# Kernel optimization log

Measured on AMD Instinct MI355X. Metric: run time of the kernel, lower is better.

The kernel has to match this reference:

```python
import jax, jax.numpy as jnp
import numpy as np

B, T, S, H, V, L = 64, 60, 60, 512, 32000, 2
NEG = -1.0e9  # matches torch mask value -1000000000.0


def setup_inputs() -> dict:
    key = jax.random.key(0)
    ks = jax.random.split(key, 12)
    sc = 0.05
    return {
        "indices": jax.random.randint(ks[0], (B, T), 0, V),
        "enc_output": jax.random.normal(ks[1], (B, S, H), dtype=jnp.float32),
        "de_lens": jax.random.randint(ks[2], (B,), 1, S + 1),
        "emb": jax.random.normal(ks[3], (V, H), dtype=jnp.float32) * sc,
        "w_ih": jax.random.normal(ks[4], (L, 4 * H, H), dtype=jnp.float32) * sc,
        "w_hh": jax.random.normal(ks[5], (L, 4 * H, H), dtype=jnp.float32) * sc,
        "b_ih": jnp.zeros((L, 4 * H), dtype=jnp.float32),
        "b_hh": jnp.zeros((L, 4 * H), dtype=jnp.float32),
        "lin_w": jax.random.normal(ks[6], (L, H, 2 * H), dtype=jnp.float32) * sc,
        "lin_b": jnp.zeros((L, H), dtype=jnp.float32),
        "out_w": jax.random.normal(ks[7], (V, H), dtype=jnp.float32) * sc,
        "out_b": jnp.zeros((V,), dtype=jnp.float32),
    }


def _lstm_seq(x, w_ih, w_hh, b_ih, b_hh):
    # x: [B,T,H] -> hidden states [B,T,H]; torch gate order i,f,g,o
    xg = jnp.einsum('bth,gh->btg', x, w_ih) + b_ih  # [B,T,4H]
    h0 = jnp.zeros((x.shape[0], w_hh.shape[1]), x.dtype)

    def step(carry, xg_t):
        h, c = carry
        g = xg_t + h @ w_hh.T + b_hh
        i, f, gg, o = jnp.split(g, 4, axis=-1)
        c = jax.nn.sigmoid(f) * c + jax.nn.sigmoid(i) * jnp.tanh(gg)
        h = jax.nn.sigmoid(o) * jnp.tanh(c)
        return (h, c), h

    _, hs = jax.lax.scan(step, (h0, h0), jnp.swapaxes(xg, 0, 1))
    return jnp.swapaxes(hs, 0, 1)


def reference(indices, enc_output, de_lens, emb, w_ih, w_hh, b_ih, b_hh,
              lin_w, lin_b, out_w, out_b):
    # additive length mask over encoder positions: [B,S]
    mask = jnp.where(jnp.arange(S)[None, :] < de_lens[:, None], 0.0, NEG).astype(enc_output.dtype)
    x = emb[indices]  # [B,T,H]
    for l in range(L):
        dec = _lstm_seq(x, w_ih[l], w_hh[l], b_ih[l], b_hh[l])  # [B,T,H]
        scores = jnp.einsum('bth,bsh->bts', dec, enc_output) + mask[:, None, :]
        probs = jax.nn.softmax(scores, axis=-1)
        attn = jnp.einsum('bts,bsh->bth', probs, enc_output)
        cat = jnp.concatenate([dec, attn], axis=-1)  # [B,T,2H]
        x = jnp.einsum('btk,hk->bth', cat, lin_w[l]) + lin_b[l]
    return jnp.einsum('bth,vh->btv', x, out_w) + out_b  # [B,T,V]
```

## Files before the change

### kernel.cpp

```cpp
#include <hip/hip_runtime.h>
#include <hip/hip_bf16.h>
#include <math.h>

#define B_ 64
#define T_ 60
#define S_ 60
#define H_ 512
#define V_ 32000
#define L_ 2
#define BT_ (B_*T_)
#define LDSROW 40

typedef __attribute__((ext_vector_type(8))) short short8;
typedef __attribute__((ext_vector_type(4))) float f32x4;
typedef __attribute__((ext_vector_type(4))) unsigned int u32x4;

__device__ __forceinline__ short f2bf(float x) {
  __hip_bfloat16 h = __float2bfloat16(x);
  return __builtin_bit_cast(short, h);
}
__device__ __forceinline__ float bf2f(short s) {
  unsigned int u = ((unsigned int)(unsigned short)s) << 16;
  return __builtin_bit_cast(float, u);
}
__device__ __forceinline__ float sigm(float x) { return 1.f / (1.f + __expf(-x)); }
__device__ __forceinline__ float tanh_(float x) {
  float e = __expf(-2.f * fabsf(x));
  float t = (1.f - e) / (1.f + e);
  return x >= 0.f ? t : -t;
}

__device__ __forceinline__ void ld4g(const char* p, u32x4* q, bool llc) {
  if (llc)
    asm volatile("global_load_dwordx4 %0, %4, off sc0 sc1\n\t"
                 "global_load_dwordx4 %1, %4, off offset:16 sc0 sc1\n\t"
                 "global_load_dwordx4 %2, %4, off offset:32 sc0 sc1\n\t"
                 "global_load_dwordx4 %3, %4, off offset:48 sc0 sc1"
                 : "=v"(q[0]), "=v"(q[1]), "=v"(q[2]), "=v"(q[3]) : "v"(p));
  else
    asm volatile("global_load_dwordx4 %0, %4, off sc0\n\t"
                 "global_load_dwordx4 %1, %4, off offset:16 sc0\n\t"
                 "global_load_dwordx4 %2, %4, off offset:32 sc0\n\t"
                 "global_load_dwordx4 %3, %4, off offset:48 sc0"
                 : "=v"(q[0]), "=v"(q[1]), "=v"(q[2]), "=v"(q[3]) : "v"(p));
}

#define LDSBAR() do { \
    asm volatile("s_waitcnt lgkmcnt(0)" ::: "memory"); \
    __builtin_amdgcn_s_barrier(); \
    __builtin_amdgcn_sched_barrier(0); \
  } while (0)

__global__ __launch_bounds__(256) void convbf_k(const float* __restrict__ src,
                                                short* __restrict__ dst) {
  int g = blockIdx.x * 256 + threadIdx.x;
  const float* s = src + (size_t)g * 8;
  float4 v0 = *(const float4*)s, v1 = *(const float4*)(s + 4);
  short8 o;
  o[0]=f2bf(v0.x); o[1]=f2bf(v0.y); o[2]=f2bf(v0.z); o[3]=f2bf(v0.w);
  o[4]=f2bf(v1.x); o[5]=f2bf(v1.y); o[6]=f2bf(v1.z); o[7]=f2bf(v1.w);
  *(short8*)(dst + (size_t)g * 8) = o;
}

__global__ __launch_bounds__(256) void pack_whh_k(const float* __restrict__ whh,
                                                  short* __restrict__ pk) {
  int idx = blockIdx.x * 256 + threadIdx.x;
  int l = idx >> 17, rem = idx & 131071;
  int n = rem >> 6, k8 = rem & 63;
  int g = n >> 9, j = n & 511;
  int np = (j >> 4) * 64 + g * 16 + (j & 15);
  const float* src = whh + ((size_t)l * 2048 + n) * 512 + k8 * 8;
  float4 v0 = *(const float4*)src, v1 = *(const float4*)(src + 4);
  short8 o;
  o[0]=f2bf(v0.x); o[1]=f2bf(v0.y); o[2]=f2bf(v0.z); o[3]=f2bf(v0.w);
  o[4]=f2bf(v1.x); o[5]=f2bf(v1.y); o[6]=f2bf(v1.z); o[7]=f2bf(v1.w);
  size_t dst = (size_t)l * (2048 * 512) + ((size_t)((np >> 4) * 64 + k8)) * 128 + (np & 15) * 8;
  *(short8*)(pk + dst) = o;
}

__global__ __launch_bounds__(256) void embed_k(const int* __restrict__ idx,
                                               const float* __restrict__ emb,
                                               float* __restrict__ x) {
  int e = blockIdx.x * 256 + threadIdx.x;
  int bt = e >> 9, h = e & (H_ - 1);
  int row = idx[bt];
  x[e] = emb[(size_t)row * H_ + h];
}

template<bool XPOSE>
__global__ __launch_bounds__(256) void gemm_a32_k(
    const float* __restrict__ A, const float* __restrict__ Bw,
    const float* __restrict__ bias1, const float* __restrict__ bias2,
    float* __restrict__ C, short* __restrict__ Cbf, int M, int N, int K) {
  __shared__ short Ahs[128 * LDSROW];
  __shared__ short Als[128 * LDSROW];
  __shared__ short Bs[128 * LDSROW];
  int tid = threadIdx.x;
  int bm = blockIdx.y * 128, bn = blockIdx.x * 128;
  int wid = tid >> 6, lane = tid & 63;
  int wr = wid >> 1, wc = wid & 1;
  int lrow = lane & 15, lk = (lane >> 4) * 8;
  f32x4 acc[4][4];
#pragma unroll
  for (int i = 0; i < 4; ++i)
#pragma unroll
    for (int j = 0; j < 4; ++j) acc[i][j] = (f32x4){0.f, 0.f, 0.f, 0.f};

  int srow = tid >> 2, scol = (tid & 3) * 8;

  for (int k0 = 0; k0 < K; k0 += 32) {
#pragma unroll
    for (int it = 0; it < 2; ++it) {
      int r = srow + it * 64;
      const float* ap = A + (size_t)(bm + r) * K + k0 + scol;
      float4 a0 = *(const float4*)ap, a1 = *(const float4*)(ap + 4);
      float av[8] = {a0.x,a0.y,a0.z,a0.w,a1.x,a1.y,a1.z,a1.w};
      short8 hv, lv;
#pragma unroll
      for (int e = 0; e < 8; ++e) {
        short h = f2bf(av[e]);
        hv[e] = h;
        lv[e] = f2bf(av[e] - bf2f(h));
      }
      *(short8*)(Ahs + r * LDSROW + scol) = hv;
      *(short8*)(Als + r * LDSROW + scol) = lv;
      const float* bp = Bw + (size_t)(bn + r) * K + k0 + scol;
      float4 b0 = *(const float4*)bp, b1 = *(const float4*)(bp + 4);
      short8 bv;
      bv[0]=f2bf(b0.x); bv[1]=f2bf(b0.y); bv[2]=f2bf(b0.z); bv[3]=f2bf(b0.w);
      bv[4]=f2bf(b1.x); bv[5]=f2bf(b1.y); bv[6]=f2bf(b1.z); bv[7]=f2bf(b1.w);
      *(short8*)(Bs + r * LDSROW + scol) = bv;
    }
    __syncthreads();
    short8 ah[4], al[4], bfr[4];
#pragma unroll
    for (int i = 0; i < 4; ++i) {
      ah[i] = *(const short8*)(Ahs + (wr * 64 + i * 16 + lrow) * LDSROW + lk);
      al[i] = *(const short8*)(Als + (wr * 64 + i * 16 + lrow) * LDSROW + lk);
    }
#pragma unroll
    for (int j = 0; j < 4; ++j)
      bfr[j] = *(const short8*)(Bs + (wc * 64 + j * 16 + lrow) * LDSROW + lk);
#pragma unroll
    for (int i = 0; i < 4; ++i)
#pragma unroll
      for (int j = 0; j < 4; ++j) {
        acc[i][j] = __builtin_amdgcn_mfma_f32_16x16x32_bf16(ah[i], bfr[j], acc[i][j], 0, 0, 0);
        acc[i][j] = __builtin_amdgcn_mfma_f32_16x16x32_bf16(al[i], bfr[j], acc[i][j], 0, 0, 0);
      }
    __syncthreads();
  }

#pragma unroll
  for (int j = 0; j < 4; ++j) {
    int col = bn + wc * 64 + j * 16 + lrow;
    float bv = bias1[col] + (bias2 ? bias2[col] : 0.f);
#pragma unroll
    for (int i = 0; i < 4; ++i) {
#pragma unroll
      for (int r = 0; r < 4; ++r) {
        int row = bm + wr * 64 + i * 16 + (lane >> 4) * 4 + r;
        float v = acc[i][j][r] + bv;
        if (XPOSE) {
          int b = row / T_, t = row - b * T_;
          int g = col >> 9, jg = col & 511;
          int c8 = b >> 3, bloc = b & 7, q = jg >> 6;
          int nploc = ((jg >> 4) & 3) * 64 + g * 16 + (jg & 15);
          C[(((size_t)t * 64 + q * 8 + c8) * 8 + bloc) * 256 + nploc] = v;
        } else {
          C[(size_t)row * N + col] = v;
          if (Cbf) Cbf[(size_t)row * N + col] = f2bf(v);
        }
      }
    }
  }
}

__global__ __launch_bounds__(256) void gemm_bb_k(
    const short* __restrict__ A, const short* __restrict__ Bbf,
    const float* __restrict__ bias, float* __restrict__ C) {
  const int N = V_, K = H_;
  int n = blockIdx.x;
  int xcd = n & 7, pos = n >> 3;
  int base = (xcd < 4) ? xcd * 938 : 4 * 938 + (xcd - 4) * 937;
  int wg = base + pos;
  int bm = (wg % 30) * 128;
  int bn = (wg / 30) * 128;

  __shared__ short As[128 * LDSROW];
  __shared__ short Bs[128 * LDSROW];
  int tid = threadIdx.x;
  int wid = tid >> 6, lane = tid & 63;
  int wr = wid >> 1, wc = wid & 1;
  int lrow = lane & 15, lk = (lane >> 4) * 8;
  f32x4 acc[4][4];
#pragma unroll
  for (int i = 0; i < 4; ++i)
#pragma unroll
    for (int j = 0; j < 4; ++j) acc[i][j] = (f32x4){0.f, 0.f, 0.f, 0.f};

  int srow = tid >> 2, scol = (tid & 3) * 8;

  for (int k0 = 0; k0 < K; k0 += 32) {
#pragma unroll
    for (int it = 0; it < 2; ++it) {
      int r = srow + it * 64;
      short8 av = *(const short8*)(A + (size_t)(bm + r) * K + k0 + scol);
      *(short8*)(As + r * LDSROW + scol) = av;
      short8 bv = *(const short8*)(Bbf + (size_t)(bn + r) * K + k0 + scol);
      *(short8*)(Bs + r * LDSROW + scol) = bv;
    }
    __syncthreads();
    short8 af[4], bfr[4];
#pragma unroll
    for (int i = 0; i < 4; ++i)
      af[i] = *(const short8*)(As + (wr * 64 + i * 16 + lrow) * LDSROW + lk);
#pragma unroll
    for (int j = 0; j < 4; ++j)
      bfr[j] = *(const short8*)(Bs + (wc * 64 + j * 16 + lrow) * LDSROW + lk);
#pragma unroll
    for (int i = 0; i < 4; ++i)
#pragma unroll
      for (int j = 0; j < 4; ++j)
        acc[i][j] = __builtin_amdgcn_mfma_f32_16x16x32_bf16(af[i], bfr[j], acc[i][j], 0, 0, 0);
    __syncthreads();
  }

#pragma unroll
  for (int j = 0; j < 4; ++j) {
    int col = bn + wc * 64 + j * 16 + lrow;
    float bv = bias[col];
#pragma unroll
    for (int i = 0; i < 4; ++i)
#pragma unroll
      for (int r = 0; r < 4; ++r) {
        int row = bm + wr * 64 + i * 16 + (lane >> 4) * 4 + r;
        C[(size_t)row * N + col] = acc[i][j][r] + bv;
      }
  }
}

__global__ __launch_bounds__(512, 2) void lstm_seq_k(
    const float* __restrict__ xg,
    const short* __restrict__ whh_pk,
    char* __restrict__ hx,
    float* __restrict__ dec) {
  __shared__ short hhi[16][520];
  __shared__ short hlo[16][520];
  __shared__ float gates[256][20];
  const int tid = threadIdx.x;
  const int bid = blockIdx.x;
  const int c = bid & 7, q = bid >> 3;
  const int w = tid >> 6, lane = tid & 63;
  const int lr = lane & 15, lkg = lane >> 4;

  for (int i = tid; i < 16 * 520; i += 512) {
    ((short*)hhi)[i] = 0;
    ((short*)hlo)[i] = 0;
  }

  short8 wreg[2][16];
#pragma unroll
  for (int nt = 0; nt < 2; ++nt)
#pragma unroll
    for (int kt = 0; kt < 16; ++kt)
      wreg[nt][kt] = *(const short8*)(whh_pk +
          ((size_t)((q * 16 + w * 2 + nt) * 64 + kt * 4 + lkg)) * 128 + lr * 8);

  const int bloc_e = tid & 7;
  const int p_e = (tid >> 3) & 31;
  const int j0 = p_e * 2;
  float cc0 = 0.f, cc1 = 0.f;

  char* grp = hx + (size_t)c * 65536;
  __syncthreads();

  for (int t = 0; t < T_; ++t) {
    const unsigned tgt = (unsigned)t;
    const char* pth = grp + (size_t)(t & 1) * 32768 + tid * 64;
    u32x4 qg[4];
    ld4g(pth, qg, false);
    for (unsigned a = 0;; ++a) {
      asm volatile("s_waitcnt vmcnt(0)" ::: "memory");
      __builtin_amdgcn_sched_barrier(0);
      unsigned bad = (qg[0][2] ^ tgt) | (qg[1][2] ^ tgt) |
                     (qg[2][2] ^ tgt) | (qg[3][2] ^ tgt);
      if (!bad) break;
      __builtin_amdgcn_s_sleep(1);
      ld4g(pth, qg, (a & 1) != 0);
    }
    u32x4 hiv = {qg[0][0], qg[1][0], qg[2][0], qg[3][0]};
    u32x4 lov = {qg[0][1], qg[1][1], qg[2][1], qg[3][1]};
    *(u32x4*)(&hhi[tid >> 6][(tid & 63) * 8]) = hiv;
    *(u32x4*)(&hlo[tid >> 6][(tid & 63) * 8]) = lov;
    LDSBAR();

    f32x4 acc[2];
    acc[0] = (f32x4){0.f, 0.f, 0.f, 0.f};
    acc[1] = (f32x4){0.f, 0.f, 0.f, 0.f};
#pragma unroll
    for (int kt = 0; kt < 16; ++kt) {
      short8 ah = *(const short8*)(&hhi[lr][kt * 32 + lkg * 8]);
      short8 al = *(const short8*)(&hlo[lr][kt * 32 + lkg * 8]);
#pragma unroll
      for (int nt = 0; nt < 2; ++nt) {
        acc[nt] = __builtin_amdgcn_mfma_f32_16x16x32_bf16(ah, wreg[nt][kt], acc[nt], 0, 0, 0);
        acc[nt] = __builtin_amdgcn_mfma_f32_16x16x32_bf16(al, wreg[nt][kt], acc[nt], 0, 0, 0);
      }
    }
#pragma unroll
    for (int nt = 0; nt < 2; ++nt)
      *(f32x4*)(&gates[(w * 2 + nt) * 16 + lr][lkg * 4]) = acc[nt];
    LDSBAR();

    if (tid < 256) {
      const float* xb = xg + ((size_t)t * 64 + bid) * 2048 + bloc_e * 256;
      float2 xv[4];
      int rw0 = (j0 >> 4) * 64 + (j0 & 15);
#pragma unroll
      for (int g = 0; g < 4; ++g)
        xv[g] = *(const float2*)(xb + rw0 + g * 16);
      float gv0[4], gv1[4];
#pragma unroll
      for (int g = 0; g < 4; ++g) {
        int rw = rw0 + g * 16;
        gv0[g] = gates[rw][bloc_e] + xv[g].x;
        gv1[g] = gates[rw + 1][bloc_e] + xv[g].y;
      }
      float cn0 = sigm(gv0[1]) * cc0 + sigm(gv0[0]) * tanh_(gv0[2]);
      float hn0 = sigm(gv0[3]) * tanh_(cn0);
      cc0 = cn0;
      float cn1 = sigm(gv1[1]) * cc1 + sigm(gv1[0]) * tanh_(gv1[2]);
      float hn1 = sigm(gv1[3]) * tanh_(cn1);
      cc1 = cn1;
      short hi0 = f2bf(hn0), hi1 = f2bf(hn1);
      short lo0 = f2bf(hn0 - bf2f(hi0)), lo1 = f2bf(hn1 - bf2f(hi1));
      u32x4 hv;
      hv[0] = (unsigned)(unsigned short)hi0 | ((unsigned)(unsigned short)hi1 << 16);
      hv[1] = (unsigned)(unsigned short)lo0 | ((unsigned)(unsigned short)lo1 << 16);
      hv[2] = tgt + 1u;
      hv[3] = tgt + 1u;
      char* pb = grp + (size_t)((t + 1) & 1) * 32768 +
                 ((size_t)(bloc_e * 256 + q * 32 + p_e)) * 16;
      asm volatile("global_store_dwordx4 %0, %1, off sc0" :: "v"(pb), "v"(hv) : "memory");
      asm volatile("global_store_dwordx4 %0, %1, off sc0 sc1" :: "v"(pb), "v"(hv) : "memory");
      float2 dv; dv.x = hn0; dv.y = hn1;
      *(float2*)(dec + ((size_t)(c * 8 + bloc_e) * T_ + t) * H_ + q * 64 + j0) = dv;
    }
    LDSBAR();
  }
}

__global__ __launch_bounds__(256) void attn_k(const float* __restrict__ dec,
                                              const float* __restrict__ enc,
                                              const int* __restrict__ lens,
                                              float* __restrict__ cat) {
  int bt = blockIdx.x;
  int b = bt / T_;
  __shared__ float dsh[H_];
  __shared__ float p[64];
  int tid = threadIdx.x;
  dsh[tid] = dec[(size_t)bt * H_ + tid];
  dsh[tid + 256] = dec[(size_t)bt * H_ + tid + 256];
  __syncthreads();
  int wid = tid >> 6, lane = tid & 63;
  int len = lens[b];
  for (int s = wid; s < S_; s += 4) {
    const float* er = enc + ((size_t)(b * S_ + s)) * H_ + lane * 8;
    float4 e0 = *(const float4*)er, e1 = *(const float4*)(er + 4);
    const float* dr = dsh + lane * 8;
    float sum = e0.x*dr[0] + e0.y*dr[1] + e0.z*dr[2] + e0.w*dr[3]
              + e1.x*dr[4] + e1.y*dr[5] + e1.z*dr[6] + e1.w*dr[7];
#pragma unroll
    for (int off = 32; off > 0; off >>= 1) sum += __shfl_down(sum, off);
    if (lane == 0) p[s] = sum + (s < len ? 0.f : -1.0e9f);
  }
  __syncthreads();
  if (wid == 0) {
    float v = (lane < S_) ? p[lane] : -INFINITY;
    float m = v;
#pragma unroll
    for (int off = 32; off > 0; off >>= 1) m = fmaxf(m, __shfl_down(m, off));
    m = __shfl(m, 0);
    float e = (lane < S_) ? expf(v - m) : 0.f;
    float ssum = e;
#pragma unroll
    for (int off = 32; off > 0; off >>= 1) ssum += __shfl_down(ssum, off);
    ssum = __shfl(ssum, 0);
    if (lane < S_) p[lane] = e / ssum;
  }
  __syncthreads();
  int h = tid * 2;
  float a0 = 0.f, a1 = 0.f;
  for (int s = 0; s < S_; ++s) {
    float ps = p[s];
    const float* er = enc + ((size_t)(b * S_ + s)) * H_ + h;
    a0 += ps * er[0];
    a1 += ps * er[1];
  }
  size_t base = (size_t)bt * (2 * H_);
  cat[base + h]          = dsh[h];
  cat[base + h + 1]      = dsh[h + 1];
  cat[base + H_ + h]     = a0;
  cat[base + H_ + h + 1] = a1;
}

extern "C" void kernel_launch(void* const* d_in, const int* in_sizes, int n_in,
                              void* d_out, int out_size, void* d_ws, size_t ws_size,
                              hipStream_t stream) {
  (void)in_sizes; (void)n_in; (void)out_size; (void)ws_size;
  const int*   indices = (const int*)d_in[0];
  const float* enc     = (const float*)d_in[1];
  const int*   de_lens = (const int*)d_in[2];
  const float* emb     = (const float*)d_in[3];
  const float* w_ih    = (const float*)d_in[4];
  const float* w_hh    = (const float*)d_in[5];
  const float* b_ih    = (const float*)d_in[6];
  const float* b_hh    = (const float*)d_in[7];
  const float* lin_w   = (const float*)d_in[8];
  const float* lin_b   = (const float*)d_in[9];
  const float* out_w   = (const float*)d_in[10];
  const float* out_b   = (const float*)d_in[11];
  float* outp = (float*)d_out;

  char* ws = (char*)d_ws;
  size_t off = 0;
  auto alloc = [&](size_t bytes) -> void* {
    void* p = ws + off; off += (bytes + 255) & ~(size_t)255; return p;
  };
  float* x      = (float*)alloc((size_t)BT_ * H_ * 4);
  float* xg     = (float*)alloc((size_t)BT_ * 4 * H_ * 4);
  float* dec    = (float*)alloc((size_t)BT_ * H_ * 4);
  float* cat    = (float*)alloc((size_t)BT_ * 2 * H_ * 4);
  short* ow_bf  = (short*)alloc((size_t)V_ * H_ * 2);
  short* whh_pk = (short*)alloc((size_t)L_ * 4 * H_ * H_ * 2);
  short* x_bf   = (short*)alloc((size_t)BT_ * H_ * 2);
  char*  hx     = (char*)alloc((size_t)8 * 2 * 32768);

  convbf_k<<<V_ * H_ / 8 / 256, 256, 0, stream>>>(out_w, ow_bf);
  pack_whh_k<<<L_ * 2048 * 64 / 256, 256, 0, stream>>>(w_hh, whh_pk);
  embed_k<<<BT_ * H_ / 256, 256, 0, stream>>>(indices, emb, x);

  for (int l = 0; l < L_; ++l) {
    gemm_a32_k<true><<<dim3(4 * H_ / 128, BT_ / 128), 256, 0, stream>>>(
        x, w_ih + (size_t)l * 4 * H_ * H_, b_ih + l * 4 * H_, b_hh + l * 4 * H_,
        xg, nullptr, BT_, 4 * H_, H_);
    hipMemsetAsync(hx, 0, (size_t)8 * 2 * 32768, stream);
    lstm_seq_k<<<64, 512, 0, stream>>>(
        xg, whh_pk + (size_t)l * 4 * H_ * H_, hx, dec);
    attn_k<<<BT_, 256, 0, stream>>>(dec, enc, de_lens, cat);
    gemm_a32_k<false><<<dim3(H_ / 128, BT_ / 128), 256, 0, stream>>>(
        cat, lin_w + (size_t)l * H_ * 2 * H_, lin_b + l * H_, nullptr,
        x, (l == L_ - 1) ? x_bf : nullptr, BT_, H_, 2 * H_);
  }

  gemm_bb_k<<<30 * (V_ / 128), 256, 0, stream>>>(x_bf, ow_bf, out_b, outp);
}
```

Before: 1.084 ms.

## Double K-tile depth in output GEMM and use nontemporal stores for logits

The vocab-projection GEMM now stages 64-wide K slices into LDS (padded row stride 72) instead of 32, which halves the number of barrier pairs and global load rounds per tile and issues two MFMA k-steps per stage. The fp32 logits output, about 490MB, is written with nontemporal global stores through inline asm so the streaming write is meant to bypass cache retention. The larger LDS footprint may lower occupancy, and the inline asm store carries no waitcnt handling, relying on the kernel end to drain the stores.

```diff
diff --git a/kernel.cpp b/kernel.cpp
--- a/kernel.cpp
+++ b/kernel.cpp
@@ -10,6 +10,7 @@
 #define L_ 2
 #define BT_ (B_*T_)
 #define LDSROW 40
+#define LDSROW2 72
 
 typedef __attribute__((ext_vector_type(8))) short short8;
 typedef __attribute__((ext_vector_type(4))) float f32x4;
@@ -187,42 +188,50 @@
   int bm = (wg % 30) * 128;
   int bn = (wg / 30) * 128;
 
-  __shared__ short As[128 * LDSROW];
-  __shared__ short Bs[128 * LDSROW];
+  __shared__ short As[128 * LDSROW2];
+  __shared__ short Bs[128 * LDSROW2];
   int tid = threadIdx.x;
   int wid = tid >> 6, lane = tid & 63;
   int wr = wid >> 1, wc = wid & 1;
-  int lrow = lane & 15, lk = (lane >> 4) * 8;
+  int lrow = lane & 15;
   f32x4 acc[4][4];
 #pragma unroll
   for (int i = 0; i < 4; ++i)
 #pragma unroll
     for (int j = 0; j < 4; ++j) acc[i][j] = (f32x4){0.f, 0.f, 0.f, 0.f};
 
-  int srow = tid >> 2, scol = (tid & 3) * 8;
-
-  for (int k0 = 0; k0 < K; k0 += 32) {
+  int srow = tid >> 2, scol = (tid & 3) * 16;
+
+  for (int k0 = 0; k0 < K; k0 += 64) {
 #pragma unroll
     for (int it = 0; it < 2; ++it) {
       int r = srow + it * 64;
-      short8 av = *(const short8*)(A + (size_t)(bm + r) * K + k0 + scol);
-      *(short8*)(As + r * LDSROW + scol) = av;
-      short8 bv = *(const short8*)(Bbf + (size_t)(bn + r) * K + k0 + scol);
-      *(short8*)(Bs + r * LDSROW + scol) = bv;
+      const short* ap = A + (size_t)(bm + r) * K + k0 + scol;
+      short8 a0 = *(const short8*)ap, a1 = *(const short8*)(ap + 8);
+      *(short8*)(As + r * LDSROW2 + scol) = a0;
+      *(short8*)(As + r * LDSROW2 + scol + 8) = a1;
+      const short* bp = Bbf + (size_t)(bn + r) * K + k0 + scol;
+      short8 b0 = *(const short8*)bp, b1 = *(const short8*)(bp + 8);
+      *(short8*)(Bs + r * LDSROW2 + scol) = b0;
+      *(short8*)(Bs + r * LDSROW2 + scol + 8) = b1;
     }
     __syncthreads();
-    short8 af[4], bfr[4];
-#pragma unroll
-    for (int i = 0; i < 4; ++i)
-      af[i] = *(const short8*)(As + (wr * 64 + i * 16 + lrow) * LDSROW + lk);
-#pragma unroll
-    for (int j = 0; j < 4; ++j)
-      bfr[j] = *(const short8*)(Bs + (wc * 64 + j * 16 + lrow) * LDSROW + lk);
-#pragma unroll
-    for (int i = 0; i < 4; ++i)
+#pragma unroll
+    for (int kk = 0; kk < 2; ++kk) {
+      int lk = kk * 32 + (lane >> 4) * 8;
+      short8 af[4], bfr[4];
+#pragma unroll
+      for (int i = 0; i < 4; ++i)
+        af[i] = *(const short8*)(As + (wr * 64 + i * 16 + lrow) * LDSROW2 + lk);
 #pragma unroll
       for (int j = 0; j < 4; ++j)
-        acc[i][j] = __builtin_amdgcn_mfma_f32_16x16x32_bf16(af[i], bfr[j], acc[i][j], 0, 0, 0);
+        bfr[j] = *(const short8*)(Bs + (wc * 64 + j * 16 + lrow) * LDSROW2 + lk);
+#pragma unroll
+      for (int i = 0; i < 4; ++i)
+#pragma unroll
+        for (int j = 0; j < 4; ++j)
+          acc[i][j] = __builtin_amdgcn_mfma_f32_16x16x32_bf16(af[i], bfr[j], acc[i][j], 0, 0, 0);
+    }
     __syncthreads();
   }
 
@@ -235,7 +244,9 @@
 #pragma unroll
       for (int r = 0; r < 4; ++r) {
         int row = bm + wr * 64 + i * 16 + (lane >> 4) * 4 + r;
-        C[(size_t)row * N + col] = acc[i][j][r] + bv;
+        float v = acc[i][j][r] + bv;
+        float* cp = C + (size_t)row * N + col;
+        asm volatile("global_store_dword %0, %1, off nt" :: "v"(cp), "v"(v) : "memory");
       }
   }
 }
```

After: 974.3 us. 1.11x faster.
